# Kernel tuning notes

Measured on AMD Instinct MI355X. Metric: run time of the kernel, lower is better.

## Reference

```python
import jax, jax.numpy as jnp
import numpy as np

B, S, D = 2, 2048, 2048
H, KVH, HD = 16, 4, 128
I = 8192
EPS = 1e-6
SCALE = HD ** -0.5
NEG = -1e9


def rms_norm(x, w):
    xf = x.astype(jnp.float32)
    var = jnp.mean(xf * xf, axis=-1, keepdims=True)
    return (w * (xf * jax.lax.rsqrt(var + EPS)).astype(x.dtype))


def rope(x, cos_f, sin_f):
    # x: (B, h, S, HD); cos_f/sin_f: (B, 1, S, HD//2). Interleaved pairs.
    xp = x.reshape(*x.shape[:-1], HD // 2, 2)
    xr, xi = xp[..., 0], xp[..., 1]
    rr = cos_f * xr - sin_f * xi
    ri = sin_f * xr + cos_f * xi
    return jnp.stack([rr, ri], axis=-1).reshape(x.shape)


def setup_inputs() -> dict:
    key = jax.random.key(0)
    ks = jax.random.split(key, 12)
    inp = {
        "hidden_states": jax.random.normal(ks[0], (B, S, D), jnp.float32),
        "cos": jax.random.normal(ks[1], (B, S, HD), jnp.float32),
        "sin": jax.random.normal(ks[2], (B, S, HD), jnp.float32),
    }
    # additive causal mask (B,1,S,S)
    causal = jnp.tril(jnp.ones((S, S), jnp.bool_))
    inp["attention_mask"] = jnp.where(causal, 0.0, NEG).astype(jnp.float32)[None, None].repeat(B, 0)
    sc = 0.02
    inp["wq"] = jax.random.normal(ks[3], (H * HD, D), jnp.float32) * sc
    inp["wk"] = jax.random.normal(ks[4], (KVH * HD, D), jnp.float32) * sc
    inp["wv"] = jax.random.normal(ks[5], (KVH * HD, D), jnp.float32) * sc
    inp["wo"] = jax.random.normal(ks[6], (D, H * HD), jnp.float32) * sc
    inp["w_gate"] = jax.random.normal(ks[7], (I, D), jnp.float32) * sc
    inp["w_up"] = jax.random.normal(ks[8], (I, D), jnp.float32) * sc
    inp["w_down"] = jax.random.normal(ks[9], (D, I), jnp.float32) * sc
    inp["ln1_w"] = jnp.ones((D,), jnp.float32)
    inp["ln2_w"] = jnp.ones((D,), jnp.float32)
    return inp


def layer_fwd(hidden_states, cos, sin, attention_mask,
              wq, wk, wv, wo, w_gate, w_up, w_down, ln1_w, ln2_w):
    residual = hidden_states
    h = rms_norm(hidden_states, ln1_w)
    # projections
    q = jnp.einsum('bsd,ed->bse', h, wq).reshape(B, S, H, HD).transpose(0, 2, 1, 3)
    k = jnp.einsum('bsd,ed->bse', h, wk).reshape(B, S, KVH, HD).transpose(0, 2, 1, 3)
    v = jnp.einsum('bsd,ed->bse', h, wv).reshape(B, S, KVH, HD).transpose(0, 2, 1, 3)
    cos_f = cos[..., :HD // 2][:, None]  # (B,1,S,HD/2)
    sin_f = sin[..., :HD // 2][:, None]
    q = rope(q, cos_f, sin_f)
    k = rope(k, cos_f, sin_f)
    # GQA: repeat_interleave kv heads
    n_rep = H // KVH
    k = jnp.repeat(k, n_rep, axis=1)
    v = jnp.repeat(v, n_rep, axis=1)
    scores = jnp.einsum('bhqd,bhkd->bhqk', q, k) * SCALE + attention_mask
    probs = jax.nn.softmax(scores.astype(jnp.float32), axis=-1).astype(q.dtype)
    attn = jnp.einsum('bhqk,bhkd->bhqd', probs, v)
    attn = attn.transpose(0, 2, 1, 3).reshape(B, S, H * HD)
    attn_out = jnp.einsum('bse,de->bsd', attn, wo)
    h = residual + attn_out
    residual = h
    m = rms_norm(h, ln2_w)
    gate = jax.nn.silu(jnp.einsum('bsd,id->bsi', m, w_gate))
    up = jnp.einsum('bsd,id->bsi', m, w_up)
    mlp_out = jnp.einsum('bsi,di->bsd', gate * up, w_down)
    return residual + mlp_out


def reference(hidden_states, cos, sin, attention_mask,
              wq, wk, wv, wo, w_gate, w_up, w_down, ln1_w, ln2_w):
    return layer_fwd(hidden_states, cos, sin, attention_mask,
                     wq, wk, wv, wo, w_gate, w_up, w_down, ln1_w, ln2_w)
```

## Files before the change

### kernel.cpp

```cpp
#include <hip/hip_runtime.h>
#include <cstdint>
#include <cstddef>

typedef unsigned short u16;
typedef short bf16x8 __attribute__((ext_vector_type(8)));
typedef float floatx4 __attribute__((ext_vector_type(4)));

__device__ __forceinline__ float b2f(u16 u) {
    union { unsigned int i; float f; } v; v.i = ((unsigned int)u) << 16; return v.f;
}
__device__ __forceinline__ u16 f2b(float f) {
    union { float f; unsigned int i; } v; v.f = f;
    unsigned int u = v.i;
    unsigned int r = (u + 0x7fffu + ((u >> 16) & 1u)) >> 16;
    return (u16)r;
}

#define GLL16(gptr, lptr)                                                          \
    __builtin_amdgcn_global_load_lds(                                              \
        (__attribute__((address_space(1))) void*)(gptr),                           \
        (__attribute__((address_space(3))) void*)(lptr), 16, 0, 0)

#define BAR_LGKM() asm volatile("s_waitcnt lgkmcnt(0)\n\ts_barrier" ::: "memory")
#define WAIT_VM8_BAR() asm volatile("s_waitcnt vmcnt(8)\n\ts_barrier" ::: "memory")
#define WAIT_VM0_BAR() asm volatile("s_waitcnt vmcnt(0)\n\ts_barrier" ::: "memory")

__global__ __launch_bounds__(256) void cvt_all(
    const float* __restrict__ wq, const float* __restrict__ wk,
    const float* __restrict__ wvp, const float* __restrict__ wo,
    const float* __restrict__ wg, const float* __restrict__ wu,
    const float* __restrict__ wd,
    u16* __restrict__ wqkv, u16* __restrict__ wob, u16* __restrict__ wgb,
    u16* __restrict__ wub, u16* __restrict__ wdb) {
    long v = (long)blockIdx.x * 256 + threadIdx.x;
    const float* s; u16* d; long o;
    if (v < 1048576)       { s = wq;  d = wqkv;           o = v; }
    else if (v < 1310720)  { s = wk;  d = wqkv + 4194304; o = v - 1048576; }
    else if (v < 1572864)  { s = wvp; d = wqkv + 5242880; o = v - 1310720; }
    else if (v < 2621440)  { s = wo;  d = wob;            o = v - 1572864; }
    else if (v < 6815744)  { s = wg;  d = wgb;            o = v - 2621440; }
    else if (v < 11010048) { s = wu;  d = wub;            o = v - 6815744; }
    else                   { s = wd;  d = wdb;            o = v - 11010048; }
    float4 x = ((const float4*)s)[o];
    u16 t[4] = { f2b(x.x), f2b(x.y), f2b(x.z), f2b(x.w) };
    ((ushort4*)d)[o] = *(const ushort4*)t;
}

__global__ __launch_bounds__(256) void rmsnorm_kernel(const float* __restrict__ x,
                                                      const float* __restrict__ w,
                                                      u16* __restrict__ out) {
    __shared__ float red[4];
    const int row = blockIdx.x;
    const float* xr = x + (size_t)row * 2048;
    const int d0 = threadIdx.x * 8;
    float4 a = *(const float4*)&xr[d0];
    float4 b = *(const float4*)&xr[d0 + 4];
    float s = a.x*a.x + a.y*a.y + a.z*a.z + a.w*a.w +
              b.x*b.x + b.y*b.y + b.z*b.z + b.w*b.w;
    #pragma unroll
    for (int m = 1; m < 64; m <<= 1) s += __shfl_xor(s, m);
    const int lane = threadIdx.x & 63, wv = threadIdx.x >> 6;
    if (lane == 0) red[wv] = s;
    __syncthreads();
    float tot = red[0] + red[1] + red[2] + red[3];
    float r = rsqrtf(tot * (1.0f / 2048.0f) + 1e-6f);
    const float* wp = w + d0;
    u16 o[8];
    o[0] = f2b(a.x * r * wp[0]); o[1] = f2b(a.y * r * wp[1]);
    o[2] = f2b(a.z * r * wp[2]); o[3] = f2b(a.w * r * wp[3]);
    o[4] = f2b(b.x * r * wp[4]); o[5] = f2b(b.y * r * wp[5]);
    o[6] = f2b(b.z * r * wp[6]); o[7] = f2b(b.w * r * wp[7]);
    *(bf16x8*)&out[(size_t)row * 2048 + d0] = *(const bf16x8*)o;
}

__global__ __launch_bounds__(256, 2) void gemm_bt(
    const u16* __restrict__ A, const u16* __restrict__ W,
    int M, int N, int K, int mode,
    u16* __restrict__ outb, float* __restrict__ outf,
    const float* __restrict__ res) {

    __shared__ __align__(16) u16 smA[2][128 * 64];
    __shared__ __align__(16) u16 smB[2][128 * 64];

    const int tid  = threadIdx.x;
    const int lane = tid & 63;
    const int c    = lane & 15;
    const int quad = lane >> 4;
    const int wv   = tid >> 6;
    const int wm   = (wv >> 1) * 64;
    const int wn   = (wv & 1) * 64;
    const int row0 = blockIdx.y * 128;
    const int col0 = blockIdx.x * 128;

    const u16* aB[4]; const u16* bB[4]; int lo[4];
    #pragma unroll
    for (int p = 0; p < 4; ++p) {
        int lin = p * 256 + tid, r = lin >> 3, g = lin & 7, sg = g ^ (r & 7);
        aB[p] = A + (size_t)(row0 + r) * K + sg * 8;
        bB[p] = W + (size_t)(col0 + r) * K + sg * 8;
        lo[p] = lin * 8;
    }
    #pragma unroll
    for (int p = 0; p < 4; ++p) { GLL16(aB[p], &smA[0][lo[p]]); GLL16(bB[p], &smB[0][lo[p]]); }

    floatx4 acc[4][4] = {};
    const int nk = K >> 6;
    for (int k = 0; k < nk; ++k) {
        BAR_LGKM();
        if (k + 1 < nk) {
            const int nb = (k + 1) & 1, ko = (k + 1) << 6;
            #pragma unroll
            for (int p = 0; p < 4; ++p) {
                GLL16(aB[p] + ko, &smA[nb][lo[p]]);
                GLL16(bB[p] + ko, &smB[nb][lo[p]]);
            }
            WAIT_VM8_BAR();
        } else {
            WAIT_VM0_BAR();
        }
        const u16* sA = smA[k & 1];
        const u16* sB = smB[k & 1];
        #pragma unroll
        for (int ks = 0; ks < 2; ++ks) {
            bf16x8 af[4], bfr[4];
            #pragma unroll
            for (int mi = 0; mi < 4; ++mi) {
                int r = wm + mi * 16 + c;
                int pos = (ks * 4 + quad) ^ (c & 7);
                af[mi] = *(const bf16x8*)&sA[r * 64 + pos * 8];
            }
            #pragma unroll
            for (int ni = 0; ni < 4; ++ni) {
                int r = wn + ni * 16 + c;
                int pos = (ks * 4 + quad) ^ (c & 7);
                bfr[ni] = *(const bf16x8*)&sB[r * 64 + pos * 8];
            }
            #pragma unroll
            for (int mi = 0; mi < 4; ++mi)
                #pragma unroll
                for (int ni = 0; ni < 4; ++ni)
                    acc[mi][ni] = __builtin_amdgcn_mfma_f32_16x16x32_bf16(
                        af[mi], bfr[ni], acc[mi][ni], 0, 0, 0);
        }
    }

    #pragma unroll
    for (int mi = 0; mi < 4; ++mi) {
        #pragma unroll
        for (int r = 0; r < 4; ++r) {
            int row = row0 + wm + mi * 16 + quad * 4 + r;
            #pragma unroll
            for (int ni = 0; ni < 4; ++ni) {
                int col = col0 + wn + ni * 16 + c;
                size_t idx = (size_t)row * N + col;
                float v = acc[mi][ni][r];
                if (mode == 0) outb[idx] = f2b(v);
                else           outf[idx] = v + res[idx];
            }
        }
    }
}

__global__ __launch_bounds__(512, 2) void mlp_gateup2(
    const u16* __restrict__ A, const u16* __restrict__ Wg,
    const u16* __restrict__ Wu, u16* __restrict__ out) {

    __shared__ __align__(16) u16 smA[2][256 * 64];
    __shared__ __align__(16) u16 smG[2][128 * 64];
    __shared__ __align__(16) u16 smU[2][128 * 64];

    const int K = 2048;
    const int tid  = threadIdx.x;
    const int lane = tid & 63;
    const int c    = lane & 15;
    const int quad = lane >> 4;
    const int wv   = tid >> 6;
    const int wm   = (wv >> 2) * 128;
    const int wn   = (wv & 3) * 32;
    const int row0 = blockIdx.y * 256;
    const int col0 = blockIdx.x * 128;

    const u16* aB[4]; int loA[4];
    #pragma unroll
    for (int p = 0; p < 4; ++p) {
        int lin = p * 512 + tid, r = lin >> 3, g = lin & 7, sg = g ^ (r & 7);
        aB[p] = A + (size_t)(row0 + r) * K + sg * 8;
        loA[p] = lin * 8;
    }
    const u16* gB[2]; const u16* uB[2]; int loGU[2];
    #pragma unroll
    for (int p = 0; p < 2; ++p) {
        int lin = p * 512 + tid, r = lin >> 3, g = lin & 7, sg = g ^ (r & 7);
        gB[p] = Wg + (size_t)(col0 + r) * K + sg * 8;
        uB[p] = Wu + (size_t)(col0 + r) * K + sg * 8;
        loGU[p] = lin * 8;
    }
    #pragma unroll
    for (int p = 0; p < 4; ++p) GLL16(aB[p], &smA[0][loA[p]]);
    #pragma unroll
    for (int p = 0; p < 2; ++p) { GLL16(gB[p], &smG[0][loGU[p]]); GLL16(uB[p], &smU[0][loGU[p]]); }

    floatx4 ag[8][2] = {}, au[8][2] = {};
    const int nk = K >> 6;
    for (int k = 0; k < nk; ++k) {
        if (k + 1 < nk) {
            const int nb = (k + 1) & 1, ko = (k + 1) << 6;
            #pragma unroll
            for (int p = 0; p < 4; ++p) GLL16(aB[p] + ko, &smA[nb][loA[p]]);
            #pragma unroll
            for (int p = 0; p < 2; ++p) {
                GLL16(gB[p] + ko, &smG[nb][loGU[p]]);
                GLL16(uB[p] + ko, &smU[nb][loGU[p]]);
            }
            WAIT_VM8_BAR();
        } else {
            WAIT_VM0_BAR();
        }
        const u16* sA = smA[k & 1];
        const u16* sG = smG[k & 1];
        const u16* sU = smU[k & 1];

        bf16x8 bg[2][2], bu[2][2];
        #pragma unroll
        for (int ks = 0; ks < 2; ++ks)
            #pragma unroll
            for (int ni = 0; ni < 2; ++ni) {
                int r = wn + ni * 16 + c;
                int pos = (ks * 4 + quad) ^ (c & 7);
                bg[ni][ks] = *(const bf16x8*)&sG[r * 64 + pos * 8];
                bu[ni][ks] = *(const bf16x8*)&sU[r * 64 + pos * 8];
            }

        #pragma unroll
        for (int ph = 0; ph < 4; ++ph) {
            bf16x8 af[2][2];
            #pragma unroll
            for (int mi = 0; mi < 2; ++mi)
                #pragma unroll
                for (int ks = 0; ks < 2; ++ks) {
                    int r = wm + (ph * 2 + mi) * 16 + c;
                    int pos = (ks * 4 + quad) ^ (c & 7);
                    af[mi][ks] = *(const bf16x8*)&sA[r * 64 + pos * 8];
                }
            __builtin_amdgcn_s_barrier();
            __builtin_amdgcn_s_setprio(1);
            #pragma unroll
            for (int mi = 0; mi < 2; ++mi)
                #pragma unroll
                for (int ks = 0; ks < 2; ++ks)
                    #pragma unroll
                    for (int ni = 0; ni < 2; ++ni) {
                        ag[ph * 2 + mi][ni] = __builtin_amdgcn_mfma_f32_16x16x32_bf16(
                            af[mi][ks], bg[ni][ks], ag[ph * 2 + mi][ni], 0, 0, 0);
                        au[ph * 2 + mi][ni] = __builtin_amdgcn_mfma_f32_16x16x32_bf16(
                            af[mi][ks], bu[ni][ks], au[ph * 2 + mi][ni], 0, 0, 0);
                    }
            __builtin_amdgcn_s_setprio(0);
            __builtin_amdgcn_s_barrier();
        }
    }

    #pragma unroll
    for (int mi = 0; mi < 8; ++mi) {
        #pragma unroll
        for (int r = 0; r < 4; ++r) {
            int row = row0 + wm + mi * 16 + quad * 4 + r;
            #pragma unroll
            for (int ni = 0; ni < 2; ++ni) {
                int col = col0 + wn + ni * 16 + c;
                float g = ag[mi][ni][r];
                float u = au[mi][ni][r];
                float sg_ = g / (1.0f + __expf(-g));
                out[(size_t)row * 8192 + col] = f2b(sg_ * u);
            }
        }
    }
}

__global__ __launch_bounds__(256) void rope_kernel(u16* __restrict__ qkv,
                                                   const float* __restrict__ cs,
                                                   const float* __restrict__ sn) {
    const int t = blockIdx.x;
    const int hh = blockIdx.y * 4 + (threadIdx.x >> 6);
    const int j = threadIdx.x & 63;
    size_t base = (size_t)t * 3072 + (hh < 16 ? hh * 128 : 2048 + (hh - 16) * 128);
    float cf = cs[(size_t)t * 128 + j];
    float sf = sn[(size_t)t * 128 + j];
    ushort2 xv = *(ushort2*)&qkv[base + 2 * j];
    float xr = b2f(xv.x), xi = b2f(xv.y);
    ushort2 ov;
    ov.x = f2b(cf * xr - sf * xi);
    ov.y = f2b(sf * xr + cf * xi);
    *(ushort2*)&qkv[base + 2 * j] = ov;
}

__global__ __launch_bounds__(256) void transpose_v(const u16* __restrict__ qkv,
                                                   u16* __restrict__ vt) {
    __shared__ __align__(16) u16 T[64][136];
    const int bkv = blockIdx.x;
    const int st = blockIdx.y;
    const int b = bkv >> 2, kvh = bkv & 3;
    const int tid = threadIdx.x;
    #pragma unroll
    for (int it = 0; it < 4; ++it) {
        int lin = it * 256 + tid;
        int sr = lin >> 4, gr = lin & 15;
        bf16x8 v = *(const bf16x8*)&qkv[((size_t)(b * 2048 + st * 64 + sr)) * 3072 +
                                        2560 + kvh * 128 + gr * 8];
        *(bf16x8*)&T[sr][gr * 8] = v;
    }
    __syncthreads();
    #pragma unroll
    for (int it = 0; it < 4; ++it) {
        int lin = it * 256 + tid;
        int n = lin >> 3, sc = lin & 7;
        u16 tmp[8];
        #pragma unroll
        for (int j = 0; j < 8; ++j) tmp[j] = T[sc * 8 + j][n];
        *(bf16x8*)&vt[((size_t)(bkv * 128 + n)) * 2048 + st * 64 + sc * 8] =
            *(const bf16x8*)tmp;
    }
}

__global__ __launch_bounds__(256, 2) void attn_kernel(const u16* __restrict__ qkv,
                                                      const u16* __restrict__ vt,
                                                      u16* __restrict__ attnb) {
    __shared__ __align__(16) u16 sK[64 * 128];
    __shared__ __align__(16) u16 sV[128 * 64];
    __shared__ __align__(16) u16 sP[4][16 * 80];

    const int tid  = threadIdx.x;
    const int lane = tid & 63;
    const int c    = lane & 15;
    const int quad = lane >> 4;
    const int wv   = tid >> 6;

    const int qt  = 31 - (int)blockIdx.x;
    const int bh  = blockIdx.y;
    const int b   = bh >> 4;
    const int h   = bh & 15;
    const int kvh = h >> 2;

    const int qrow = qt * 64 + wv * 16 + c;
    const size_t qbase = ((size_t)(b * 2048 + qrow)) * 3072 + h * 128;
    bf16x8 qf[4];
    #pragma unroll
    for (int kk = 0; kk < 4; ++kk)
        qf[kk] = *(const bf16x8*)&qkv[qbase + kk * 32 + quad * 8];

    floatx4 o[8] = {};
    float m_[4], l_[4];
    #pragma unroll
    for (int r = 0; r < 4; ++r) { m_[r] = -__builtin_inff(); l_[r] = 0.0f; }

    const float SC = 0.08838834764831845f;

    for (int kt = 0; kt <= qt; ++kt) {
        const int kv0 = kt * 64;
        __syncthreads();
        #pragma unroll
        for (int p = 0; p < 4; ++p) {
            int lin = p * 256 + tid;
            {
                int r = lin >> 4, g = lin & 15;
                int sg = g ^ (r & 7);
                const u16* gk = qkv + ((size_t)(b * 2048 + kv0 + r)) * 3072 +
                                2048 + kvh * 128 + sg * 8;
                GLL16(gk, &sK[lin * 8]);
            }
            {
                int r = lin >> 3, g = lin & 7;
                int sg = g ^ (r & 7);
                const u16* gv = vt + ((size_t)((b * 4 + kvh) * 128 + r)) * 2048 +
                                kv0 + sg * 8;
                GLL16(gv, &sV[lin * 8]);
            }
        }
        __syncthreads();

        floatx4 s[4] = {};
        #pragma unroll
        for (int kk = 0; kk < 4; ++kk) {
            #pragma unroll
            for (int ct = 0; ct < 4; ++ct) {
                int rk = ct * 16 + c;
                int pos = (kk * 4 + quad) ^ (c & 7);
                bf16x8 kf = *(const bf16x8*)&sK[rk * 128 + pos * 8];
                s[ct] = __builtin_amdgcn_mfma_f32_16x16x32_bf16(qf[kk], kf, s[ct], 0, 0, 0);
            }
        }

        const int qloc = wv * 16 + quad * 4;
        #pragma unroll
        for (int ct = 0; ct < 4; ++ct) {
            #pragma unroll
            for (int r = 0; r < 4; ++r) {
                float v = s[ct][r] * SC;
                if (kt == qt && (ct * 16 + c) > (qloc + r)) v = -__builtin_inff();
                s[ct][r] = v;
            }
        }

        float alpha[4];
        #pragma unroll
        for (int r = 0; r < 4; ++r) {
            float rm = fmaxf(fmaxf(s[0][r], s[1][r]), fmaxf(s[2][r], s[3][r]));
            rm = fmaxf(rm, __shfl_xor(rm, 1));
            rm = fmaxf(rm, __shfl_xor(rm, 2));
            rm = fmaxf(rm, __shfl_xor(rm, 4));
            rm = fmaxf(rm, __shfl_xor(rm, 8));
            float mn = fmaxf(m_[r], rm);
            alpha[r] = __expf(m_[r] - mn);
            m_[r] = mn;
        }
        #pragma unroll
        for (int r = 0; r < 4; ++r) {
            float rs = 0.0f;
            #pragma unroll
            for (int ct = 0; ct < 4; ++ct) {
                float p = __expf(s[ct][r] - m_[r]);
                s[ct][r] = p;
                rs += p;
            }
            rs += __shfl_xor(rs, 1);
            rs += __shfl_xor(rs, 2);
            rs += __shfl_xor(rs, 4);
            rs += __shfl_xor(rs, 8);
            l_[r] = l_[r] * alpha[r] + rs;
        }

        u16* sp = &sP[wv][0];
        #pragma unroll
        for (int ct = 0; ct < 4; ++ct)
            #pragma unroll
            for (int r = 0; r < 4; ++r)
                sp[(quad * 4 + r) * 80 + ct * 16 + c] = f2b(s[ct][r]);

        #pragma unroll
        for (int nt = 0; nt < 8; ++nt)
            #pragma unroll
            for (int r = 0; r < 4; ++r)
                o[nt][r] *= alpha[r];

        #pragma unroll
        for (int ks2 = 0; ks2 < 2; ++ks2) {
            bf16x8 pa = *(const bf16x8*)&sp[c * 80 + ks2 * 32 + quad * 8];
            #pragma unroll
            for (int nt = 0; nt < 8; ++nt) {
                int rv = nt * 16 + c;
                int pos = (ks2 * 4 + quad) ^ (c & 7);
                bf16x8 vb = *(const bf16x8*)&sV[rv * 64 + pos * 8];
                o[nt] = __builtin_amdgcn_mfma_f32_16x16x32_bf16(pa, vb, o[nt], 0, 0, 0);
            }
        }
    }

    float inv[4];
    #pragma unroll
    for (int r = 0; r < 4; ++r) inv[r] = 1.0f / l_[r];
    #pragma unroll
    for (int nt = 0; nt < 8; ++nt) {
        #pragma unroll
        for (int r = 0; r < 4; ++r) {
            int row = qt * 64 + wv * 16 + quad * 4 + r;
            int col = h * 128 + nt * 16 + c;
            attnb[((size_t)(b * 2048 + row)) * 2048 + col] = f2b(o[nt][r] * inv[r]);
        }
    }
}

extern "C" void kernel_launch(void* const* d_in, const int* in_sizes, int n_in,
                              void* d_out, int out_size, void* d_ws, size_t ws_size,
                              hipStream_t stream) {
    const float* hidden = (const float*)d_in[0];
    const float* cosp   = (const float*)d_in[1];
    const float* sinp   = (const float*)d_in[2];
    const float* wq  = (const float*)d_in[4];
    const float* wk  = (const float*)d_in[5];
    const float* wvp = (const float*)d_in[6];
    const float* wo  = (const float*)d_in[7];
    const float* wg  = (const float*)d_in[8];
    const float* wu  = (const float*)d_in[9];
    const float* wd  = (const float*)d_in[10];
    const float* ln1 = (const float*)d_in[11];
    const float* ln2 = (const float*)d_in[12];
    float* outp = (float*)d_out;

    char* ws = (char*)d_ws;
    size_t off = 0;
    auto alloc = [&](size_t bytes) {
        void* p = ws + off;
        off += (bytes + 255) & ~(size_t)255;
        return p;
    };
    u16* wqkv_b  = (u16*)alloc((size_t)3072 * 2048 * 2);
    u16* wo_b    = (u16*)alloc((size_t)2048 * 2048 * 2);
    u16* wg_b    = (u16*)alloc((size_t)8192 * 2048 * 2);
    u16* wu_b    = (u16*)alloc((size_t)8192 * 2048 * 2);
    u16* wd_b    = (u16*)alloc((size_t)2048 * 8192 * 2);
    u16* normed  = (u16*)alloc((size_t)4096 * 2048 * 2);
    u16* qkv     = (u16*)alloc((size_t)4096 * 3072 * 2);
    u16* vtb     = (u16*)alloc((size_t)8 * 128 * 2048 * 2);
    u16* attnb   = (u16*)alloc((size_t)4096 * 2048 * 2);
    float* h1    = (float*)alloc((size_t)4096 * 2048 * 4);
    u16* hidprod = (u16*)alloc((size_t)4096 * 8192 * 2);
    (void)ws_size; (void)in_sizes; (void)n_in; (void)out_size;

    cvt_all<<<59392, 256, 0, stream>>>(wq, wk, wvp, wo, wg, wu, wd,
                                       wqkv_b, wo_b, wg_b, wu_b, wd_b);

    rmsnorm_kernel<<<4096, 256, 0, stream>>>(hidden, ln1, normed);

    gemm_bt<<<dim3(24, 32), 256, 0, stream>>>(normed, wqkv_b, 4096, 3072, 2048, 0,
                                              qkv, nullptr, nullptr);

    rope_kernel<<<dim3(4096, 5), 256, 0, stream>>>(qkv, cosp, sinp);
    transpose_v<<<dim3(8, 32), 256, 0, stream>>>(qkv, vtb);
    attn_kernel<<<dim3(32, 32), 256, 0, stream>>>(qkv, vtb, attnb);

    gemm_bt<<<dim3(16, 32), 256, 0, stream>>>(attnb, wo_b, 4096, 2048, 2048, 1,
                                              nullptr, h1, hidden);

    rmsnorm_kernel<<<4096, 256, 0, stream>>>(h1, ln2, normed);

    mlp_gateup2<<<dim3(64, 16), 512, 0, stream>>>(normed, wg_b, wu_b, hidprod);

    gemm_bt<<<dim3(16, 32), 256, 0, stream>>>(hidprod, wd_b, 4096, 2048, 8192, 1,
                                              nullptr, outp, h1);
}
```

Baseline: 1.115 ms.

## Interleave next-tile global-to-LDS loads across MFMA phases in gate/up MLP kernel

The gate/up GEMM kernel no longer issues all next-tile global_load_lds operations at the top of each K iteration. It spreads them across the four compute phases (gate, up, then two halves of A), each followed by a partial vmcnt wait and a barrier. It also changes the A-row assignment per thread so A can be staged in halves. The aim is to overlap memory traffic with MFMA work more evenly and drop the bulk wait at the start of each iteration. The risk is that the fine-grained vmcnt counts are wrong and expose races, or that the extra barriers add stalls.

```diff
diff --git a/kernel.cpp b/kernel.cpp
--- a/kernel.cpp
+++ b/kernel.cpp
@@ -24,6 +24,7 @@
 #define BAR_LGKM() asm volatile("s_waitcnt lgkmcnt(0)\n\ts_barrier" ::: "memory")
 #define WAIT_VM8_BAR() asm volatile("s_waitcnt vmcnt(8)\n\ts_barrier" ::: "memory")
 #define WAIT_VM0_BAR() asm volatile("s_waitcnt vmcnt(0)\n\ts_barrier" ::: "memory")
+#define WAITV_BAR(n) asm volatile("s_waitcnt vmcnt(" #n ")\n\ts_barrier" ::: "memory")
 
 __global__ __launch_bounds__(256) void cvt_all(
     const float* __restrict__ wq, const float* __restrict__ wk,
@@ -161,7 +162,43 @@
     }
 }
 
-__global__ __launch_bounds__(512, 2) void mlp_gateup2(
+#define STAGE_G(buf, ko) { GLL16(gSrc0 + (ko), &smG[buf][guD0]); GLL16(gSrc1 + (ko), &smG[buf][guD1]); }
+#define STAGE_U(buf, ko) { GLL16(uSrc0 + (ko), &smU[buf][guD0]); GLL16(uSrc1 + (ko), &smU[buf][guD1]); }
+#define STAGE_A2(buf, ko, j0, j1)                                              \
+    { GLL16(aSrc + (size_t)(j0) * 32 * 2048 + (ko), &smA[buf][aDst + (j0) * 32 * 64]); \
+      GLL16(aSrc + (size_t)(j1) * 32 * 2048 + (ko), &smA[buf][aDst + (j1) * 32 * 64]); }
+
+#define MLP_PHASE(ph, STAGE_STMT, WAIT_STMT)                                   \
+    {                                                                          \
+        bf16x8 af[2][2];                                                       \
+        _Pragma("unroll")                                                      \
+        for (int mi = 0; mi < 2; ++mi)                                         \
+            _Pragma("unroll")                                                  \
+            for (int ks = 0; ks < 2; ++ks) {                                   \
+                int r = wm + (ph) * 32 + mi * 16 + c;                          \
+                int pos = (ks * 4 + quad) ^ (c & 7);                           \
+                af[mi][ks] = *(const bf16x8*)&sA[r * 64 + pos * 8];            \
+            }                                                                  \
+        STAGE_STMT;                                                            \
+        __builtin_amdgcn_s_barrier();                                          \
+        asm volatile("s_waitcnt lgkmcnt(0)" ::: "memory");                     \
+        __builtin_amdgcn_s_setprio(1);                                         \
+        _Pragma("unroll")                                                      \
+        for (int mi = 0; mi < 2; ++mi)                                         \
+            _Pragma("unroll")                                                  \
+            for (int ks = 0; ks < 2; ++ks)                                     \
+                _Pragma("unroll")                                              \
+                for (int ni = 0; ni < 2; ++ni) {                               \
+                    ag[(ph) * 2 + mi][ni] = __builtin_amdgcn_mfma_f32_16x16x32_bf16( \
+                        af[mi][ks], bg[ni][ks], ag[(ph) * 2 + mi][ni], 0, 0, 0);     \
+                    au[(ph) * 2 + mi][ni] = __builtin_amdgcn_mfma_f32_16x16x32_bf16( \
+                        af[mi][ks], bu[ni][ks], au[(ph) * 2 + mi][ni], 0, 0, 0);     \
+                }                                                              \
+        __builtin_amdgcn_s_setprio(0);                                         \
+        WAIT_STMT;                                                             \
+    }
+
+__global__ __launch_bounds__(512, 2) void mlp_gateup3(
     const u16* __restrict__ A, const u16* __restrict__ Wg,
     const u16* __restrict__ Wu, u16* __restrict__ out) {
 
@@ -180,45 +217,36 @@
     const int row0 = blockIdx.y * 256;
     const int col0 = blockIdx.x * 128;
 
-    const u16* aB[4]; int loA[4];
-    #pragma unroll
-    for (int p = 0; p < 4; ++p) {
-        int lin = p * 512 + tid, r = lin >> 3, g = lin & 7, sg = g ^ (r & 7);
-        aB[p] = A + (size_t)(row0 + r) * K + sg * 8;
-        loA[p] = lin * 8;
-    }
-    const u16* gB[2]; const u16* uB[2]; int loGU[2];
-    #pragma unroll
-    for (int p = 0; p < 2; ++p) {
-        int lin = p * 512 + tid, r = lin >> 3, g = lin & 7, sg = g ^ (r & 7);
-        gB[p] = Wg + (size_t)(col0 + r) * K + sg * 8;
-        uB[p] = Wu + (size_t)(col0 + r) * K + sg * 8;
-        loGU[p] = lin * 8;
-    }
-    #pragma unroll
-    for (int p = 0; p < 4; ++p) GLL16(aB[p], &smA[0][loA[p]]);
-    #pragma unroll
-    for (int p = 0; p < 2; ++p) { GLL16(gB[p], &smG[0][loGU[p]]); GLL16(uB[p], &smU[0][loGU[p]]); }
+    const int rloc = tid >> 3, g = tid & 7;
+    const int Rbase = (tid < 256) ? rloc : (96 + rloc);
+    const int sgA = g ^ (rloc & 7);
+    const u16* aSrc = A + (size_t)(row0 + Rbase) * K + sgA * 8;
+    const int aDst = Rbase * 64 + g * 8;
+
+    const u16* gSrc0; const u16* gSrc1; const u16* uSrc0; const u16* uSrc1;
+    int guD0, guD1;
+    {
+        int lin = tid, r = lin >> 3, gg = lin & 7, sg = gg ^ (r & 7);
+        gSrc0 = Wg + (size_t)(col0 + r) * K + sg * 8;
+        uSrc0 = Wu + (size_t)(col0 + r) * K + sg * 8;
+        guD0 = lin * 8;
+        lin = 512 + tid; r = lin >> 3; gg = lin & 7; sg = gg ^ (r & 7);
+        gSrc1 = Wg + (size_t)(col0 + r) * K + sg * 8;
+        uSrc1 = Wu + (size_t)(col0 + r) * K + sg * 8;
+        guD1 = lin * 8;
+    }
+
+    STAGE_G(0, 0); STAGE_U(0, 0); STAGE_A2(0, 0, 0, 1); STAGE_A2(0, 0, 2, 3);
+    WAITV_BAR(3);
 
     floatx4 ag[8][2] = {}, au[8][2] = {};
     const int nk = K >> 6;
     for (int k = 0; k < nk; ++k) {
-        if (k + 1 < nk) {
-            const int nb = (k + 1) & 1, ko = (k + 1) << 6;
-            #pragma unroll
-            for (int p = 0; p < 4; ++p) GLL16(aB[p] + ko, &smA[nb][loA[p]]);
-            #pragma unroll
-            for (int p = 0; p < 2; ++p) {
-                GLL16(gB[p] + ko, &smG[nb][loGU[p]]);
-                GLL16(uB[p] + ko, &smU[nb][loGU[p]]);
-            }
-            WAIT_VM8_BAR();
-        } else {
-            WAIT_VM0_BAR();
-        }
-        const u16* sA = smA[k & 1];
-        const u16* sG = smG[k & 1];
-        const u16* sU = smU[k & 1];
+        const int cur = k & 1, nb = cur ^ 1;
+        const int ko = (k + 1) << 6;
+        const u16* sA = smA[cur];
+        const u16* sG = smG[cur];
+        const u16* sU = smU[cur];
 
         bf16x8 bg[2][2], bu[2][2];
         #pragma unroll
@@ -231,32 +259,16 @@
                 bu[ni][ks] = *(const bf16x8*)&sU[r * 64 + pos * 8];
             }
 
-        #pragma unroll
-        for (int ph = 0; ph < 4; ++ph) {
-            bf16x8 af[2][2];
-            #pragma unroll
-            for (int mi = 0; mi < 2; ++mi)
-                #pragma unroll
-                for (int ks = 0; ks < 2; ++ks) {
-                    int r = wm + (ph * 2 + mi) * 16 + c;
-                    int pos = (ks * 4 + quad) ^ (c & 7);
-                    af[mi][ks] = *(const bf16x8*)&sA[r * 64 + pos * 8];
-                }
-            __builtin_amdgcn_s_barrier();
-            __builtin_amdgcn_s_setprio(1);
-            #pragma unroll
-            for (int mi = 0; mi < 2; ++mi)
-                #pragma unroll
-                for (int ks = 0; ks < 2; ++ks)
-                    #pragma unroll
-                    for (int ni = 0; ni < 2; ++ni) {
-                        ag[ph * 2 + mi][ni] = __builtin_amdgcn_mfma_f32_16x16x32_bf16(
-                            af[mi][ks], bg[ni][ks], ag[ph * 2 + mi][ni], 0, 0, 0);
-                        au[ph * 2 + mi][ni] = __builtin_amdgcn_mfma_f32_16x16x32_bf16(
-                            af[mi][ks], bu[ni][ks], au[ph * 2 + mi][ni], 0, 0, 0);
-                    }
-            __builtin_amdgcn_s_setprio(0);
-            __builtin_amdgcn_s_barrier();
+        if (k + 1 < nk) {
+            MLP_PHASE(0, STAGE_G(nb, ko),        WAITV_BAR(4));
+            MLP_PHASE(1, STAGE_U(nb, ko),        WAITV_BAR(5));
+            MLP_PHASE(2, STAGE_A2(nb, ko, 0, 1), WAITV_BAR(6));
+            MLP_PHASE(3, STAGE_A2(nb, ko, 2, 3), WAITV_BAR(3));
+        } else {
+            MLP_PHASE(0, , WAITV_BAR(2));
+            MLP_PHASE(1, , WAITV_BAR(1));
+            MLP_PHASE(2, , WAITV_BAR(0));
+            MLP_PHASE(3, , );
         }
     }
 
@@ -268,10 +280,10 @@
             #pragma unroll
             for (int ni = 0; ni < 2; ++ni) {
                 int col = col0 + wn + ni * 16 + c;
-                float g = ag[mi][ni][r];
-                float u = au[mi][ni][r];
-                float sg_ = g / (1.0f + __expf(-g));
-                out[(size_t)row * 8192 + col] = f2b(sg_ * u);
+                float gv = ag[mi][ni][r];
+                float uv = au[mi][ni][r];
+                float sg_ = gv / (1.0f + __expf(-gv));
+                out[(size_t)row * 8192 + col] = f2b(sg_ * uv);
             }
         }
     }
@@ -523,7 +535,7 @@
 
     rmsnorm_kernel<<<4096, 256, 0, stream>>>(h1, ln2, normed);
 
-    mlp_gateup2<<<dim3(64, 16), 512, 0, stream>>>(normed, wg_b, wu_b, hidprod);
+    mlp_gateup3<<<dim3(64, 16), 512, 0, stream>>>(normed, wg_b, wu_b, hidprod);
 
     gemm_bt<<<dim3(16, 32), 256, 0, stream>>>(hidprod, wd_b, 4096, 2048, 8192, 1,
                                               nullptr, outp, h1);
```

Measured after the change: 1.085 ms. 2.7% less time.
